# Kernel optimization log

Hardware: AMD Instinct MI355X
Metric: run time of the kernel (lower is better)

Reference implementation:

```python
import jax, jax.numpy as jnp
import numpy as np

N_NODES = 20000
N_EDGES = 80000
D = 128       # in_dim_node == in_dim_edge == hidden dims
ITERS = 15    # mp_iterations
EPS = 1e-5    # torch LayerNorm default eps


def _mlp(h, W0, b0, W1, b1, W2, b2, gamma, beta):
    """Linear-ReLU-Linear-ReLU-Linear-LayerNorm (hidden_layers=2)."""
    h = jax.nn.relu(h @ W0 + b0)
    h = jax.nn.relu(h @ W1 + b1)
    h = h @ W2 + b2
    mu = jnp.mean(h, axis=-1, keepdims=True)
    var = jnp.var(h, axis=-1, keepdims=True)
    return gamma * (h - mu) * jax.lax.rsqrt(var + EPS) + beta


def setup_inputs() -> dict:
    key = jax.random.key(0)
    ks = iter(jax.random.split(key, 32))

    def lin(fi, fo):
        bnd = 1.0 / np.sqrt(fi)
        W = jax.random.uniform(next(ks), (ITERS, fi, fo), minval=-bnd, maxval=bnd, dtype=jnp.float32)
        b = jax.random.uniform(next(ks), (ITERS, fo), minval=-bnd, maxval=bnd, dtype=jnp.float32)
        return W, b

    x = jax.random.normal(next(ks), (N_NODES, D), dtype=jnp.float32)
    edge_attr = jax.random.normal(next(ks), (N_EDGES, D), dtype=jnp.float32)
    edge_index = jax.random.randint(next(ks), (2, N_EDGES), 0, N_NODES)

    eW0, eB0 = lin(3 * D, D)   # edge MLP input = cat(src, dest, edge) = 384
    eW1, eB1 = lin(D, D)
    eW2, eB2 = lin(D, D)
    nW0, nB0 = lin(2 * D, D)   # node MLP input = cat(x, agg) = 256
    nW1, nB1 = lin(D, D)
    nW2, nB2 = lin(D, D)
    ones = jnp.ones((ITERS, D), jnp.float32)
    zeros = jnp.zeros((ITERS, D), jnp.float32)

    return dict(x=x, edge_attr=edge_attr,
                eW0=eW0, eB0=eB0, eW1=eW1, eB1=eB1, eW2=eW2, eB2=eB2, eG=ones, eBeta=zeros,
                nW0=nW0, nB0=nB0, nW1=nW1, nB1=nB1, nW2=nW2, nB2=nB2, nG=ones, nBeta=zeros,
                edge_index=edge_index)


def reference(x, edge_attr, eW0, eB0, eW1, eB1, eW2, eB2, eG, eBeta,
              nW0, nB0, nW1, nB1, nW2, nB2, nG, nBeta, edge_index):
    row, col = edge_index[0], edge_index[1]
    n = x.shape[0]
    params = (eW0, eB0, eW1, eB1, eW2, eB2, eG, eBeta,
              nW0, nB0, nW1, nB1, nW2, nB2, nG, nBeta)

    def step(carry, p):
        xc, ec = carry
        (ew0, eb0, ew1, eb1, ew2, eb2, eg, ebt,
         nw0, nb0, nw1, nb1, nw2, nb2, ng, nbt) = p
        # EdgeProcessor: gather + MLP, then FullResidualConnection (add previous)
        e_in = jnp.concatenate([xc[row], xc[col], ec], axis=-1)        # [E, 3D]
        ec = _mlp(e_in, ew0, eb0, ew1, eb1, ew2, eb2, eg, ebt) + ec
        # NodeProcessor: scatter_sum over destination nodes + MLP + residual
        agg = jax.ops.segment_sum(ec, col, num_segments=n)             # [N, D]
        n_in = jnp.concatenate([xc, agg], axis=-1)                     # [N, 2D]
        xc = _mlp(n_in, nw0, nb0, nw1, nb1, nw2, nb2, ng, nbt) + xc
        return (xc, ec), None

    (x, edge_attr), _ = jax.lax.scan(step, (x, edge_attr), params)
    return x, edge_attr
```

## Files before the change

### kernel.cpp

```cpp
#include <hip/hip_runtime.h>
#include <hip/hip_bf16.h>

typedef __hip_bfloat16 bf16;
typedef __attribute__((ext_vector_type(8))) short short8;
typedef __attribute__((ext_vector_type(4))) float f32x4;

#define NN 20000
#define NE 80000
#define DD 128
#define NITER 15
#define HSTRIDE 136

__device__ inline void gload16(const void* g, void* l) {
  __builtin_amdgcn_global_load_lds(
      (const __attribute__((address_space(1))) void*)g,
      (__attribute__((address_space(3))) void*)l, 16, 0, 0);
}

__device__ inline float bfbits2f(unsigned int hi16) {
  union { unsigned int u; float f; } c; c.u = hi16; return c.f;
}

__global__ void detect_kernel(const unsigned short* __restrict__ p, int nhalf,
                              int* __restrict__ flag) {
  __shared__ int cs[256], ct[256];
  const int t = threadIdx.x;
  int sane = 0, tot = 0;
  for (int i = 2 * t; i < nhalf; i += 512) {
    unsigned short v = p[i];
    int e = (v >> 7) & 0xFF;
    tot++;
    if (v == 0 || (e >= 80 && e <= 170)) sane++;
  }
  cs[t] = sane; ct[t] = tot;
  __syncthreads();
  for (int o = 128; o > 0; o >>= 1) {
    if (t < o) { cs[t] += cs[t + o]; ct[t] += ct[t + o]; }
    __syncthreads();
  }
  if (t == 0) *flag = (cs[0] * 10 > ct[0] * 7) ? 1 : 0;
}

__global__ void in2fb_kernel(const void* __restrict__ src, float* __restrict__ dstf,
                             bf16* __restrict__ dstb, int n, const int* __restrict__ flag) {
  int i = blockIdx.x * 256 + threadIdx.x;
  if (i < n) {
    float v = (*flag) ? (float)((const bf16*)src)[i] : ((const float*)src)[i];
    dstf[i] = v;
    dstb[i] = (bf16)v;
  }
}

__global__ void in2f_kernel(const void* __restrict__ src, float* __restrict__ dst,
                            int n, const int* __restrict__ flag) {
  int i = blockIdx.x * 256 + threadIdx.x;
  if (i < n) {
    dst[i] = (*flag) ? (float)((const bf16*)src)[i] : ((const float*)src)[i];
  }
}

__global__ void w2t_kernel(const void* __restrict__ W, bf16* __restrict__ Wt,
                           int K, const int* __restrict__ flag) {
  int i = blockIdx.x * 256 + threadIdx.x;
  int total = NITER * K * DD;
  if (i < total) {
    float v = (*flag) ? (float)((const bf16*)W)[i] : ((const float*)W)[i];
    int t = i / (K * DD);
    int rem = i - t * K * DD;
    int k = rem >> 7;
    int n = rem & 127;
    Wt[(size_t)t * K * DD + (size_t)n * K + k] = (bf16)v;
  }
}

__global__ void outw_kernel(const float* __restrict__ xf, const float* __restrict__ ef,
                            void* __restrict__ out, const int* __restrict__ flag) {
  int i = blockIdx.x * 256 + threadIdx.x;
  const int nx = NN * DD, total = (NN + NE) * DD;
  if (i < total) {
    float v = (i < nx) ? xf[i] : ef[i - nx];
    if (*flag) ((bf16*)out)[i] = (bf16)v;
    else       ((float*)out)[i] = v;
  }
}

template<int K0, int AMODE>
__global__ __launch_bounds__(256, 3) void fused_mlp(
    const bf16*  __restrict__ S0b,
    const bf16*  __restrict__ S1b,
    const int*   __restrict__ eidx,
    const bf16*  __restrict__ W0t,
    const bf16*  __restrict__ W1t,
    const bf16*  __restrict__ W2t,
    const float* __restrict__ b0,
    const float* __restrict__ b1,
    const float* __restrict__ b2,
    const float* __restrict__ gamma,
    const float* __restrict__ beta,
    float*       __restrict__ stf,
    bf16*        __restrict__ stb,
    int M)
{
  __shared__ __align__(16) bf16 Bls[2][128 * 32];
  __shared__ __align__(16) bf16 Hls[128 * HSTRIDE];

  const int tid  = threadIdx.x;
  const int lane = tid & 63;
  const int wv   = tid >> 6;
  const int l15  = lane & 15, quad = lane >> 4;
  const int m0   = blockIdx.x * 128;

  const int scol = tid >> 2;
  const int sk8  = (tid & 3) * 8;

  int rowm[2], ir[2], ic[2];
#pragma unroll
  for (int mi = 0; mi < 2; mi++) {
    rowm[mi] = min(m0 + wv * 32 + mi * 16 + l15, M - 1);
    if (AMODE == 1) { ir[mi] = eidx[rowm[mi]]; ic[mi] = eidx[NE + rowm[mi]]; }
  }

  auto dmaW = [&](const bf16* W, int K, int kk, int buf) {
    gload16(W + (size_t)scol * K + kk + sk8,        &Bls[buf][scol * 32 + sk8]);
    gload16(W + (size_t)(scol + 64) * K + kk + sk8, &Bls[buf][(scol + 64) * 32 + sk8]);
  };
  auto gatherA = [&](int kk, short8 a[2]) {
    const int ks = (kk & 127) + quad * 8;
#pragma unroll
    for (int mi = 0; mi < 2; mi++) {
      const bf16* base;
      if (AMODE == 1) {
        const int seg = kk >> 7;
        base = (seg == 0) ? S0b + (size_t)ir[mi] * DD
             : (seg == 1) ? S0b + (size_t)ic[mi] * DD
                          : S1b + (size_t)rowm[mi] * DD;
      } else {
        base = (kk >> 7) ? S1b + (size_t)rowm[mi] * DD
                         : S0b + (size_t)rowm[mi] * DD;
      }
      a[mi] = *(const short8*)(base + ks);
    }
  };

  f32x4 acc[2][8];
  auto zacc = [&]() {
#pragma unroll
    for (int i = 0; i < 2; i++)
#pragma unroll
      for (int j = 0; j < 8; j++) acc[i][j] = (f32x4){0.f, 0.f, 0.f, 0.f};
  };
  auto slabMfmaA = [&](const short8 a[2], int buf) {
    short8 bfr[8];
#pragma unroll
    for (int ni = 0; ni < 8; ni++)
      bfr[ni] = *(const short8*)&Bls[buf][(ni * 16 + l15) * 32 + quad * 8];
#pragma unroll
    for (int mi = 0; mi < 2; mi++)
#pragma unroll
      for (int ni = 0; ni < 8; ni++)
        acc[mi][ni] = __builtin_amdgcn_mfma_f32_16x16x32_bf16(a[mi], bfr[ni], acc[mi][ni], 0, 0, 0);
  };
  auto slabMfmaH = [&](int kk, int buf) {
    short8 a[2], bfr[8];
#pragma unroll
    for (int mi = 0; mi < 2; mi++)
      a[mi] = *(const short8*)&Hls[(wv * 32 + mi * 16 + l15) * HSTRIDE + kk + quad * 8];
#pragma unroll
    for (int ni = 0; ni < 8; ni++)
      bfr[ni] = *(const short8*)&Bls[buf][(ni * 16 + l15) * 32 + quad * 8];
#pragma unroll
    for (int mi = 0; mi < 2; mi++)
#pragma unroll
      for (int ni = 0; ni < 8; ni++)
        acc[mi][ni] = __builtin_amdgcn_mfma_f32_16x16x32_bf16(a[mi], bfr[ni], acc[mi][ni], 0, 0, 0);
  };
  auto writeH = [&](const float* bias) {
    float bv[8];
#pragma unroll
    for (int ni = 0; ni < 8; ni++) bv[ni] = bias[ni * 16 + l15];
#pragma unroll
    for (int mi = 0; mi < 2; mi++)
#pragma unroll
      for (int r = 0; r < 4; r++) {
        const int row = wv * 32 + mi * 16 + quad * 4 + r;
#pragma unroll
        for (int ni = 0; ni < 8; ni++)
          Hls[row * HSTRIDE + ni * 16 + l15] = (bf16)fmaxf(acc[mi][ni][r] + bv[ni], 0.f);
      }
  };

  constexpr int NS1 = K0 / 32;

  zacc();
  short8 aCur[2], aNxt[2];
  dmaW(W0t, K0, 0, 0);
  gatherA(0, aCur);
  __syncthreads();
#pragma unroll
  for (int s = 0; s < NS1; s++) {
    if (s + 1 < NS1) {
      dmaW(W0t, K0, (s + 1) * 32, (s + 1) & 1);
      gatherA((s + 1) * 32, aNxt);
    } else {
      dmaW(W1t, 128, 0, NS1 & 1);
    }
    slabMfmaA(aCur, s & 1);
    __syncthreads();
    aCur[0] = aNxt[0]; aCur[1] = aNxt[1];
  }
  writeH(b0);
  __syncthreads();

  zacc();
#pragma unroll
  for (int s = 0; s < 4; s++) {
    if (s < 3) dmaW(W1t, 128, (s + 1) * 32, (NS1 + s + 1) & 1);
    else       dmaW(W2t, 128, 0,            (NS1 + 4) & 1);
    slabMfmaH(s * 32, (NS1 + s) & 1);
    __syncthreads();
  }
  writeH(b1);
  __syncthreads();

  zacc();
#pragma unroll
  for (int s = 0; s < 4; s++) {
    if (s < 3) dmaW(W2t, 128, (s + 1) * 32, (NS1 + 4 + s + 1) & 1);
    slabMfmaH(s * 32, (NS1 + 4 + s) & 1);
    if (s < 3) __syncthreads();
  }

  float bv[8], gv[8], btv[8];
#pragma unroll
  for (int ni = 0; ni < 8; ni++) {
    const int col = ni * 16 + l15;
    bv[ni] = b2[col]; gv[ni] = gamma[col]; btv[ni] = beta[col];
  }
#pragma unroll
  for (int mi = 0; mi < 2; mi++)
#pragma unroll
    for (int r = 0; r < 4; r++) {
      float a = 0.f, bq = 0.f;
#pragma unroll
      for (int ni = 0; ni < 8; ni++) {
        const float v = acc[mi][ni][r] + bv[ni];
        a += v; bq += v * v;
      }
#pragma unroll
      for (int off = 1; off < 16; off <<= 1) {
        a  += __shfl_xor(a, off);
        bq += __shfl_xor(bq, off);
      }
      const float mu = a * (1.0f / 128.0f);
      const float var = fmaxf(bq * (1.0f / 128.0f) - mu * mu, 0.0f);
      const float rs = rsqrtf(var + 1e-5f);
      const int m = m0 + wv * 32 + mi * 16 + quad * 4 + r;
      if (m < M) {
#pragma unroll
        for (int ni = 0; ni < 8; ni++) {
          const int col = ni * 16 + l15;
          const float v = acc[mi][ni][r] + bv[ni];
          const float lnv = (v - mu) * rs * gv[ni] + btv[ni];
          const size_t idx = (size_t)m * DD + col;
          const float nv = lnv + stf[idx];
          stf[idx] = nv;
          stb[idx] = (bf16)nv;
        }
      }
    }
}

__global__ void zero_kernel(int* __restrict__ p, int n) {
  int i = blockIdx.x * 256 + threadIdx.x;
  if (i < n) p[i] = 0;
}

__global__ void hist_kernel(const int* __restrict__ eidx, int* __restrict__ counts) {
  int e = blockIdx.x * 256 + threadIdx.x;
  if (e < NE) atomicAdd(&counts[eidx[NE + e]], 1);
}

__global__ void scan_kernel(const int* __restrict__ counts, int* __restrict__ offs,
                            int* __restrict__ cursor) {
  __shared__ int sums[1024];
  const int t = threadIdx.x;
  const int base = t * 20;
  int local[20];
  int s = 0;
  for (int i = 0; i < 20; i++) {
    int idx = base + i;
    int c = (idx < NN) ? counts[idx] : 0;
    local[i] = s; s += c;
  }
  sums[t] = s;
  __syncthreads();
  for (int off = 1; off < 1024; off <<= 1) {
    int v = 0;
    if (t >= off) v = sums[t - off];
    __syncthreads();
    if (t >= off) sums[t] += v;
    __syncthreads();
  }
  int excl = (t == 0) ? 0 : sums[t - 1];
  for (int i = 0; i < 20; i++) {
    int idx = base + i;
    if (idx < NN) { offs[idx] = excl + local[i]; cursor[idx] = 0; }
  }
  if (t == 1023) offs[NN] = sums[1023];
}

__global__ void fill_kernel(const int* __restrict__ eidx, const int* __restrict__ offs,
                            int* __restrict__ cursor, int* __restrict__ sorted) {
  int e = blockIdx.x * 256 + threadIdx.x;
  if (e < NE) {
    int n = eidx[NE + e];
    int p = atomicAdd(&cursor[n], 1);
    sorted[offs[n] + p] = e;
  }
}

__global__ void aggregate_kernel(const bf16* __restrict__ eb, const int* __restrict__ offs,
                                 const int* __restrict__ sorted, bf16* __restrict__ aggb) {
  const int node = blockIdx.x * 4 + (threadIdx.x >> 6);
  const int lane = threadIdx.x & 63;
  if (node >= NN) return;
  const int s = offs[node], t = offs[node + 1];
  float a0 = 0.f, a1 = 0.f;
  for (int i = s; i < t; i++) {
    const int e = sorted[i];
    unsigned int v = *(const unsigned int*)(eb + (size_t)e * DD + 2 * lane);
    a0 += bfbits2f(v << 16);
    a1 += bfbits2f(v & 0xFFFF0000u);
  }
  bf16 o0 = (bf16)a0, o1 = (bf16)a1;
  unsigned int pack = (unsigned int)(*(unsigned short*)&o0)
                    | ((unsigned int)(*(unsigned short*)&o1) << 16);
  *(unsigned int*)(aggb + (size_t)node * DD + 2 * lane) = pack;
}

extern "C" void kernel_launch(void* const* d_in, const int* in_sizes, int n_in,
                              void* d_out, int out_size, void* d_ws, size_t ws_size,
                              hipStream_t stream) {
  const void* x_in = d_in[0];
  const void* e_in = d_in[1];
  const void* eW0 = d_in[2];
  const void* eB0 = d_in[3];
  const void* eW1 = d_in[4];
  const void* eB1 = d_in[5];
  const void* eW2 = d_in[6];
  const void* eB2 = d_in[7];
  const void* eG  = d_in[8];
  const void* eBt = d_in[9];
  const void* nW0 = d_in[10];
  const void* nB0 = d_in[11];
  const void* nW1 = d_in[12];
  const void* nB1 = d_in[13];
  const void* nW2 = d_in[14];
  const void* nB2 = d_in[15];
  const void* nG  = d_in[16];
  const void* nBt = d_in[17];
  const int*  eidx = (const int*)d_in[18];

  char* ws = (char*)d_ws;
  size_t off = 0;
  auto alloc = [&](size_t bytes) -> char* {
    char* p = ws + off;
    off = (off + bytes + 255) & ~(size_t)255;
    return p;
  };

  float* xf   = (float*)alloc((size_t)NN * DD * 4);
  float* ef   = (float*)alloc((size_t)NE * DD * 4);
  bf16*  xb   = (bf16*)alloc((size_t)NN * DD * 2);
  bf16*  eb   = (bf16*)alloc((size_t)NE * DD * 2);
  bf16*  aggb = (bf16*)alloc((size_t)NN * DD * 2);
  bf16*  eW0t = (bf16*)alloc((size_t)NITER * 384 * DD * 2);
  bf16*  eW1t = (bf16*)alloc((size_t)NITER * 128 * DD * 2);
  bf16*  eW2t = (bf16*)alloc((size_t)NITER * 128 * DD * 2);
  bf16*  nW0t = (bf16*)alloc((size_t)NITER * 256 * DD * 2);
  bf16*  nW1t = (bf16*)alloc((size_t)NITER * 128 * DD * 2);
  bf16*  nW2t = (bf16*)alloc((size_t)NITER * 128 * DD * 2);
  const int NB = NITER * DD;
  float* eB0f = (float*)alloc(NB * 4);
  float* eB1f = (float*)alloc(NB * 4);
  float* eB2f = (float*)alloc(NB * 4);
  float* eGf  = (float*)alloc(NB * 4);
  float* eBtf = (float*)alloc(NB * 4);
  float* nB0f = (float*)alloc(NB * 4);
  float* nB1f = (float*)alloc(NB * 4);
  float* nB2f = (float*)alloc(NB * 4);
  float* nGf  = (float*)alloc(NB * 4);
  float* nBtf = (float*)alloc(NB * 4);
  int* counts = (int*)alloc((size_t)NN * 4);
  int* cursor = (int*)alloc((size_t)NN * 4);
  int* offs   = (int*)alloc((size_t)(NN + 1) * 4);
  int* sorted = (int*)alloc((size_t)NE * 4);
  int* flag   = (int*)alloc(4);

  detect_kernel<<<1, 256, 0, stream>>>((const unsigned short*)x_in, 16384, flag);

  in2fb_kernel<<<(NN * DD + 255) / 256, 256, 0, stream>>>(x_in, xf, xb, NN * DD, flag);
  in2fb_kernel<<<(NE * DD + 255) / 256, 256, 0, stream>>>(e_in, ef, eb, NE * DD, flag);
  w2t_kernel<<<(NITER * 384 * DD + 255) / 256, 256, 0, stream>>>(eW0, eW0t, 384, flag);
  w2t_kernel<<<(NITER * 128 * DD + 255) / 256, 256, 0, stream>>>(eW1, eW1t, 128, flag);
  w2t_kernel<<<(NITER * 128 * DD + 255) / 256, 256, 0, stream>>>(eW2, eW2t, 128, flag);
  w2t_kernel<<<(NITER * 256 * DD + 255) / 256, 256, 0, stream>>>(nW0, nW0t, 256, flag);
  w2t_kernel<<<(NITER * 128 * DD + 255) / 256, 256, 0, stream>>>(nW1, nW1t, 128, flag);
  w2t_kernel<<<(NITER * 128 * DD + 255) / 256, 256, 0, stream>>>(nW2, nW2t, 128, flag);
  in2f_kernel<<<(NB + 255) / 256, 256, 0, stream>>>(eB0, eB0f, NB, flag);
  in2f_kernel<<<(NB + 255) / 256, 256, 0, stream>>>(eB1, eB1f, NB, flag);
  in2f_kernel<<<(NB + 255) / 256, 256, 0, stream>>>(eB2, eB2f, NB, flag);
  in2f_kernel<<<(NB + 255) / 256, 256, 0, stream>>>(eG,  eGf,  NB, flag);
  in2f_kernel<<<(NB + 255) / 256, 256, 0, stream>>>(eBt, eBtf, NB, flag);
  in2f_kernel<<<(NB + 255) / 256, 256, 0, stream>>>(nB0, nB0f, NB, flag);
  in2f_kernel<<<(NB + 255) / 256, 256, 0, stream>>>(nB1, nB1f, NB, flag);
  in2f_kernel<<<(NB + 255) / 256, 256, 0, stream>>>(nB2, nB2f, NB, flag);
  in2f_kernel<<<(NB + 255) / 256, 256, 0, stream>>>(nG,  nGf,  NB, flag);
  in2f_kernel<<<(NB + 255) / 256, 256, 0, stream>>>(nBt, nBtf, NB, flag);

  zero_kernel<<<(NN + 255) / 256, 256, 0, stream>>>(counts, NN);
  hist_kernel<<<(NE + 255) / 256, 256, 0, stream>>>(eidx, counts);
  scan_kernel<<<1, 1024, 0, stream>>>(counts, offs, cursor);
  fill_kernel<<<(NE + 255) / 256, 256, 0, stream>>>(eidx, offs, cursor, sorted);

  const int egrid = NE / 128;
  const int ngrid = (NN + 127) / 128;

  for (int t = 0; t < NITER; t++) {
    fused_mlp<384, 1><<<egrid, 256, 0, stream>>>(
        xb, eb, eidx,
        eW0t + (size_t)t * 384 * DD, eW1t + (size_t)t * 128 * DD, eW2t + (size_t)t * 128 * DD,
        eB0f + t * DD, eB1f + t * DD, eB2f + t * DD,
        eGf + t * DD, eBtf + t * DD, ef, eb, NE);
    aggregate_kernel<<<(NN + 3) / 4, 256, 0, stream>>>(eb, offs, sorted, aggb);
    fused_mlp<256, 2><<<ngrid, 256, 0, stream>>>(
        xb, aggb, nullptr,
        nW0t + (size_t)t * 256 * DD, nW1t + (size_t)t * 128 * DD, nW2t + (size_t)t * 128 * DD,
        nB0f + t * DD, nB1f + t * DD, nB2f + t * DD,
        nGf + t * DD, nBtf + t * DD, xf, xb, NN);
  }

  outw_kernel<<<((NN + NE) * DD + 255) / 256, 256, 0, stream>>>(xf, ef, d_out, flag);
}
```

Baseline: 1.295 ms.

## Fuse aggregation into node MLP, drop fp32 residual state, merge preprocessing kernels

```diff
diff --git a/kernel.cpp b/kernel.cpp
--- a/kernel.cpp
+++ b/kernel.cpp
@@ -21,13 +21,22 @@
   union { unsigned int u; float f; } c; c.u = hi16; return c.f;
 }
 
-__global__ void detect_kernel(const unsigned short* __restrict__ p, int nhalf,
-                              int* __restrict__ flag) {
+__device__ inline float readin(const void* p, int i, int fl) {
+  return fl ? (float)((const bf16*)p)[i] : ((const float*)p)[i];
+}
+
+__global__ void detzero_kernel(const unsigned short* __restrict__ x,
+                               int* __restrict__ counts, int* __restrict__ flag) {
+  const int bid = blockIdx.x, t = threadIdx.x;
+  if (bid < 79) {
+    int i = bid * 256 + t;
+    if (i < NN) counts[i] = 0;
+    return;
+  }
   __shared__ int cs[256], ct[256];
-  const int t = threadIdx.x;
   int sane = 0, tot = 0;
-  for (int i = 2 * t; i < nhalf; i += 512) {
-    unsigned short v = p[i];
+  for (int i = 2 * t; i < 16384; i += 512) {
+    unsigned short v = x[i];
     int e = (v >> 7) & 0xFF;
     tot++;
     if (v == 0 || (e >= 80 && e <= 170)) sane++;
@@ -41,66 +50,69 @@
   if (t == 0) *flag = (cs[0] * 10 > ct[0] * 7) ? 1 : 0;
 }
 
-__global__ void in2fb_kernel(const void* __restrict__ src, float* __restrict__ dstf,
-                             bf16* __restrict__ dstb, int n, const int* __restrict__ flag) {
-  int i = blockIdx.x * 256 + threadIdx.x;
-  if (i < n) {
-    float v = (*flag) ? (float)((const bf16*)src)[i] : ((const float*)src)[i];
-    dstf[i] = v;
-    dstb[i] = (bf16)v;
-  }
-}
-
-__global__ void in2f_kernel(const void* __restrict__ src, float* __restrict__ dst,
-                            int n, const int* __restrict__ flag) {
-  int i = blockIdx.x * 256 + threadIdx.x;
-  if (i < n) {
-    dst[i] = (*flag) ? (float)((const bf16*)src)[i] : ((const float*)src)[i];
-  }
-}
-
-__global__ void w2t_kernel(const void* __restrict__ W, bf16* __restrict__ Wt,
-                           int K, const int* __restrict__ flag) {
-  int i = blockIdx.x * 256 + threadIdx.x;
-  int total = NITER * K * DD;
-  if (i < total) {
-    float v = (*flag) ? (float)((const bf16*)W)[i] : ((const float*)W)[i];
-    int t = i / (K * DD);
-    int rem = i - t * K * DD;
-    int k = rem >> 7;
-    int n = rem & 127;
-    Wt[(size_t)t * K * DD + (size_t)n * K + k] = (bf16)v;
-  }
-}
-
-__global__ void outw_kernel(const float* __restrict__ xf, const float* __restrict__ ef,
-                            void* __restrict__ out, const int* __restrict__ flag) {
-  int i = blockIdx.x * 256 + threadIdx.x;
-  const int nx = NN * DD, total = (NN + NE) * DD;
-  if (i < total) {
-    float v = (i < nx) ? xf[i] : ef[i - nx];
-    if (*flag) ((bf16*)out)[i] = (bf16)v;
-    else       ((float*)out)[i] = v;
-  }
-}
-
-template<int K0, int AMODE>
-__global__ __launch_bounds__(256, 3) void fused_mlp(
-    const bf16*  __restrict__ S0b,
-    const bf16*  __restrict__ S1b,
-    const int*   __restrict__ eidx,
-    const bf16*  __restrict__ W0t,
-    const bf16*  __restrict__ W1t,
-    const bf16*  __restrict__ W2t,
-    const float* __restrict__ b0,
-    const float* __restrict__ b1,
+#define CX  (NN * DD)
+#define CE  (NE * DD)
+#define CW0 (NITER * 384 * DD)
+#define CW1 (NITER * 128 * DD)
+#define CNW0 (NITER * 256 * DD)
+#define CB  (NITER * DD)
+#define BX0 CX
+#define BX1 (BX0 + CE)
+#define BX7 (BX1 + CW0 + CW1 + CW1 + CNW0 + CW1 + CW1)
+#define BX8 (BX7 + 10 * CB)
+
+struct CvtP {
+  const void *x, *e;
+  const void* w[6];
+  bf16 *xb, *eb;
+  bf16* wt[6];
+  const void* bs[10];
+  float* bd[10];
+  const int* flag;
+};
+
+__global__ void convert_all(CvtP P) {
+  const int fl = *P.flag;
+  const int gstride = gridDim.x * 256;
+  for (int i = blockIdx.x * 256 + threadIdx.x; i < BX8; i += gstride) {
+    if (i < BX0) {
+      P.xb[i] = (bf16)readin(P.x, i, fl);
+    } else if (i < BX1) {
+      P.eb[i - BX0] = (bf16)readin(P.e, i - BX0, fl);
+    } else if (i < BX7) {
+      int j = i - BX1, w;
+      if (j < CW0) { w = 0; }
+      else if ((j -= CW0) < CW1) { w = 1; }
+      else if ((j -= CW1) < CW1) { w = 2; }
+      else if ((j -= CW1) < CNW0) { w = 3; }
+      else if ((j -= CNW0) < CW1) { w = 4; }
+      else { j -= CW1; w = 5; }
+      const int K = (w == 0) ? 384 : (w == 3) ? 256 : 128;
+      float v = readin(P.w[w], j, fl);
+      int it = j / (K * DD);
+      int rem = j - it * K * DD;
+      int k = rem >> 7, n = rem & 127;
+      P.wt[w][(size_t)it * K * DD + (size_t)n * K + k] = (bf16)v;
+    } else {
+      int j = i - BX7;
+      int b = j / CB, r = j - b * CB;
+      P.bd[b][r] = readin(P.bs[b], r, fl);
+    }
+  }
+}
+
+__global__ __launch_bounds__(256, 3) void edge_mlp(
+    const bf16* __restrict__ xb,
+    const bf16* eb,
+    const int*  __restrict__ eidx,
+    const bf16* __restrict__ W0t, const bf16* __restrict__ W1t,
+    const bf16* __restrict__ W2t,
+    const float* __restrict__ b0, const float* __restrict__ b1,
     const float* __restrict__ b2,
-    const float* __restrict__ gamma,
-    const float* __restrict__ beta,
-    float*       __restrict__ stf,
-    bf16*        __restrict__ stb,
-    int M)
+    const float* __restrict__ gamma, const float* __restrict__ beta,
+    bf16* st, int M)
 {
+  constexpr int K0 = 384, NS1 = 12;
   __shared__ __align__(16) bf16 Bls[2][128 * 32];
   __shared__ __align__(16) bf16 Hls[128 * HSTRIDE];
 
@@ -109,7 +121,6 @@
   const int wv   = tid >> 6;
   const int l15  = lane & 15, quad = lane >> 4;
   const int m0   = blockIdx.x * 128;
-
   const int scol = tid >> 2;
   const int sk8  = (tid & 3) * 8;
 
@@ -117,7 +128,7 @@
 #pragma unroll
   for (int mi = 0; mi < 2; mi++) {
     rowm[mi] = min(m0 + wv * 32 + mi * 16 + l15, M - 1);
-    if (AMODE == 1) { ir[mi] = eidx[rowm[mi]]; ic[mi] = eidx[NE + rowm[mi]]; }
+    ir[mi] = eidx[rowm[mi]]; ic[mi] = eidx[NE + rowm[mi]];
   }
 
   auto dmaW = [&](const bf16* W, int K, int kk, int buf) {
@@ -128,16 +139,10 @@
     const int ks = (kk & 127) + quad * 8;
 #pragma unroll
     for (int mi = 0; mi < 2; mi++) {
-      const bf16* base;
-      if (AMODE == 1) {
-        const int seg = kk >> 7;
-        base = (seg == 0) ? S0b + (size_t)ir[mi] * DD
-             : (seg == 1) ? S0b + (size_t)ic[mi] * DD
-                          : S1b + (size_t)rowm[mi] * DD;
-      } else {
-        base = (kk >> 7) ? S1b + (size_t)rowm[mi] * DD
-                         : S0b + (size_t)rowm[mi] * DD;
-      }
+      const int seg = kk >> 7;
+      const bf16* base = (seg == 0) ? xb + (size_t)ir[mi] * DD
+                       : (seg == 1) ? xb + (size_t)ic[mi] * DD
+                                    : eb + (size_t)rowm[mi] * DD;
       a[mi] = *(const short8*)(base + ks);
     }
   };
@@ -188,8 +193,6 @@
           Hls[row * HSTRIDE + ni * 16 + l15] = (bf16)fmaxf(acc[mi][ni][r] + bv[ni], 0.f);
       }
   };
-
-  constexpr int NS1 = K0 / 32;
 
   zacc();
   short8 aCur[2], aNxt[2];
@@ -262,17 +265,176 @@
           const float v = acc[mi][ni][r] + bv[ni];
           const float lnv = (v - mu) * rs * gv[ni] + btv[ni];
           const size_t idx = (size_t)m * DD + col;
-          const float nv = lnv + stf[idx];
-          stf[idx] = nv;
-          stb[idx] = (bf16)nv;
+          st[idx] = (bf16)(lnv + (float)st[idx]);
         }
       }
     }
 }
 
-__global__ void zero_kernel(int* __restrict__ p, int n) {
-  int i = blockIdx.x * 256 + threadIdx.x;
-  if (i < n) p[i] = 0;
+__global__ __launch_bounds__(256, 4) void node_mlp(
+    const bf16* xb,
+    const bf16* __restrict__ eb,
+    const int*  __restrict__ offs,
+    const int*  __restrict__ sorted,
+    const bf16* __restrict__ W0t, const bf16* __restrict__ W1t,
+    const bf16* __restrict__ W2t,
+    const float* __restrict__ b0, const float* __restrict__ b1,
+    const float* __restrict__ b2,
+    const float* __restrict__ gamma, const float* __restrict__ beta,
+    bf16* st, int M)
+{
+  constexpr int K0 = 256, NS1 = 8;
+  __shared__ __align__(16) bf16 Bls[2][128 * 32];
+  __shared__ __align__(16) bf16 Hls[64 * HSTRIDE];
+
+  const int tid  = threadIdx.x;
+  const int lane = tid & 63;
+  const int wv   = tid >> 6;
+  const int l15  = lane & 15, quad = lane >> 4;
+  const int m0   = blockIdx.x * 64;
+  const int scol = tid >> 2;
+  const int sk8  = (tid & 3) * 8;
+
+  for (int j = 0; j < 16; j++) {
+    const int n = m0 + wv * 16 + j;
+    if (n < M) {
+      const int s = offs[n], e2 = offs[n + 1];
+      float a0 = 0.f, a1 = 0.f;
+      for (int i = s; i < e2; i++) {
+        const int e = sorted[i];
+        unsigned int v = *(const unsigned int*)(eb + (size_t)e * DD + 2 * lane);
+        a0 += bfbits2f(v << 16);
+        a1 += bfbits2f(v & 0xFFFF0000u);
+      }
+      bf16 o0 = (bf16)a0, o1 = (bf16)a1;
+      unsigned int pack = (unsigned int)(*(unsigned short*)&o0)
+                        | ((unsigned int)(*(unsigned short*)&o1) << 16);
+      *(unsigned int*)&Hls[(wv * 16 + j) * HSTRIDE + 2 * lane] = pack;
+    }
+  }
+
+  const int rowm = min(m0 + wv * 16 + l15, M - 1);
+
+  auto dmaW = [&](const bf16* W, int K, int kk, int buf) {
+    gload16(W + (size_t)scol * K + kk + sk8,        &Bls[buf][scol * 32 + sk8]);
+    gload16(W + (size_t)(scol + 64) * K + kk + sk8, &Bls[buf][(scol + 64) * 32 + sk8]);
+  };
+  auto gatherA = [&](int kk, short8* a) {
+    const int ks = (kk & 127) + quad * 8;
+    if (kk < 128) *a = *(const short8*)(xb + (size_t)rowm * DD + ks);
+    else          *a = *(const short8*)&Hls[(rowm - m0) * HSTRIDE + ks];
+  };
+
+  f32x4 acc[8];
+  auto zacc = [&]() {
+#pragma unroll
+    for (int j = 0; j < 8; j++) acc[j] = (f32x4){0.f, 0.f, 0.f, 0.f};
+  };
+  auto slabMfmaA = [&](short8 a, int buf) {
+    short8 bfr[8];
+#pragma unroll
+    for (int ni = 0; ni < 8; ni++)
+      bfr[ni] = *(const short8*)&Bls[buf][(ni * 16 + l15) * 32 + quad * 8];
+#pragma unroll
+    for (int ni = 0; ni < 8; ni++)
+      acc[ni] = __builtin_amdgcn_mfma_f32_16x16x32_bf16(a, bfr[ni], acc[ni], 0, 0, 0);
+  };
+  auto slabMfmaH = [&](int kk, int buf) {
+    short8 a = *(const short8*)&Hls[(wv * 16 + l15) * HSTRIDE + kk + quad * 8];
+    short8 bfr[8];
+#pragma unroll
+    for (int ni = 0; ni < 8; ni++)
+      bfr[ni] = *(const short8*)&Bls[buf][(ni * 16 + l15) * 32 + quad * 8];
+#pragma unroll
+    for (int ni = 0; ni < 8; ni++)
+      acc[ni] = __builtin_amdgcn_mfma_f32_16x16x32_bf16(a, bfr[ni], acc[ni], 0, 0, 0);
+  };
+  auto writeH = [&](const float* bias) {
+    float bv[8];
+#pragma unroll
+    for (int ni = 0; ni < 8; ni++) bv[ni] = bias[ni * 16 + l15];
+#pragma unroll
+    for (int r = 0; r < 4; r++) {
+      const int row = wv * 16 + quad * 4 + r;
+#pragma unroll
+      for (int ni = 0; ni < 8; ni++)
+        Hls[row * HSTRIDE + ni * 16 + l15] = (bf16)fmaxf(acc[ni][r] + bv[ni], 0.f);
+    }
+  };
+
+  zacc();
+  short8 aCur, aNxt;
+  dmaW(W0t, K0, 0, 0);
+  gatherA(0, &aCur);
+  __syncthreads();
+#pragma unroll
+  for (int s = 0; s < NS1; s++) {
+    if (s + 1 < NS1) {
+      dmaW(W0t, K0, (s + 1) * 32, (s + 1) & 1);
+      gatherA((s + 1) * 32, &aNxt);
+    } else {
+      dmaW(W1t, 128, 0, NS1 & 1);
+    }
+    slabMfmaA(aCur, s & 1);
+    __syncthreads();
+    aCur = aNxt;
+  }
+  writeH(b0);
+  __syncthreads();
+
+  zacc();
+#pragma unroll
+  for (int s = 0; s < 4; s++) {
+    if (s < 3) dmaW(W1t, 128, (s + 1) * 32, (NS1 + s + 1) & 1);
+    else       dmaW(W2t, 128, 0,            (NS1 + 4) & 1);
+    slabMfmaH(s * 32, (NS1 + s) & 1);
+    __syncthreads();
+  }
+  writeH(b1);
+  __syncthreads();
+
+  zacc();
+#pragma unroll
+  for (int s = 0; s < 4; s++) {
+    if (s < 3) dmaW(W2t, 128, (s + 1) * 32, (NS1 + 4 + s + 1) & 1);
+    slabMfmaH(s * 32, (NS1 + 4 + s) & 1);
+    if (s < 3) __syncthreads();
+  }
+
+  float bv[8], gv[8], btv[8];
+#pragma unroll
+  for (int ni = 0; ni < 8; ni++) {
+    const int col = ni * 16 + l15;
+    bv[ni] = b2[col]; gv[ni] = gamma[col]; btv[ni] = beta[col];
+  }
+#pragma unroll
+  for (int r = 0; r < 4; r++) {
+    float a = 0.f, bq = 0.f;
+#pragma unroll
+    for (int ni = 0; ni < 8; ni++) {
+      const float v = acc[ni][r] + bv[ni];
+      a += v; bq += v * v;
+    }
+#pragma unroll
+    for (int off = 1; off < 16; off <<= 1) {
+      a  += __shfl_xor(a, off);
+      bq += __shfl_xor(bq, off);
+    }
+    const float mu = a * (1.0f / 128.0f);
+    const float var = fmaxf(bq * (1.0f / 128.0f) - mu * mu, 0.0f);
+    const float rs = rsqrtf(var + 1e-5f);
+    const int m = m0 + wv * 16 + quad * 4 + r;
+    if (m < M) {
+#pragma unroll
+      for (int ni = 0; ni < 8; ni++) {
+        const int col = ni * 16 + l15;
+        const float v = acc[ni][r] + bv[ni];
+        const float lnv = (v - mu) * rs * gv[ni] + btv[ni];
+        const size_t idx = (size_t)m * DD + col;
+        st[idx] = (bf16)(lnv + (float)st[idx]);
+      }
+    }
+  }
 }
 
 __global__ void hist_kernel(const int* __restrict__ eidx, int* __restrict__ counts) {
@@ -319,47 +481,21 @@
   }
 }
 
-__global__ void aggregate_kernel(const bf16* __restrict__ eb, const int* __restrict__ offs,
-                                 const int* __restrict__ sorted, bf16* __restrict__ aggb) {
-  const int node = blockIdx.x * 4 + (threadIdx.x >> 6);
-  const int lane = threadIdx.x & 63;
-  if (node >= NN) return;
-  const int s = offs[node], t = offs[node + 1];
-  float a0 = 0.f, a1 = 0.f;
-  for (int i = s; i < t; i++) {
-    const int e = sorted[i];
-    unsigned int v = *(const unsigned int*)(eb + (size_t)e * DD + 2 * lane);
-    a0 += bfbits2f(v << 16);
-    a1 += bfbits2f(v & 0xFFFF0000u);
-  }
-  bf16 o0 = (bf16)a0, o1 = (bf16)a1;
-  unsigned int pack = (unsigned int)(*(unsigned short*)&o0)
-                    | ((unsigned int)(*(unsigned short*)&o1) << 16);
-  *(unsigned int*)(aggb + (size_t)node * DD + 2 * lane) = pack;
+__global__ void outwb_kernel(const bf16* __restrict__ xb, const bf16* __restrict__ eb,
+                             void* __restrict__ out, const int* __restrict__ flag) {
+  int i = blockIdx.x * 256 + threadIdx.x;
+  const int nx = NN * DD, total = (NN + NE) * DD;
+  if (i < total) {
+    bf16 v = (i < nx) ? xb[i] : eb[i - nx];
+    if (*flag) ((bf16*)out)[i] = v;
+    else       ((float*)out)[i] = (float)v;
+  }
 }
 
 extern "C" void kernel_launch(void* const* d_in, const int* in_sizes, int n_in,
                               void* d_out, int out_size, void* d_ws, size_t ws_size,
                               hipStream_t stream) {
-  const void* x_in = d_in[0];
-  const void* e_in = d_in[1];
-  const void* eW0 = d_in[2];
-  const void* eB0 = d_in[3];
-  const void* eW1 = d_in[4];
-  const void* eB1 = d_in[5];
-  const void* eW2 = d_in[6];
-  const void* eB2 = d_in[7];
-  const void* eG  = d_in[8];
-  const void* eBt = d_in[9];
-  const void* nW0 = d_in[10];
-  const void* nB0 = d_in[11];
-  const void* nW1 = d_in[12];
-  const void* nB1 = d_in[13];
-  const void* nW2 = d_in[14];
-  const void* nB2 = d_in[15];
-  const void* nG  = d_in[16];
-  const void* nBt = d_in[17];
-  const int*  eidx = (const int*)d_in[18];
+  const int* eidx = (const int*)d_in[18];
 
   char* ws = (char*)d_ws;
   size_t off = 0;
@@ -369,76 +505,57 @@
     return p;
   };
 
-  float* xf   = (float*)alloc((size_t)NN * DD * 4);
-  float* ef   = (float*)alloc((size_t)NE * DD * 4);
-  bf16*  xb   = (bf16*)alloc((size_t)NN * DD * 2);
-  bf16*  eb   = (bf16*)alloc((size_t)NE * DD * 2);
-  bf16*  aggb = (bf16*)alloc((size_t)NN * DD * 2);
-  bf16*  eW0t = (bf16*)alloc((size_t)NITER * 384 * DD * 2);
-  bf16*  eW1t = (bf16*)alloc((size_t)NITER * 128 * DD * 2);
-  bf16*  eW2t = (bf16*)alloc((size_t)NITER * 128 * DD * 2);
-  bf16*  nW0t = (bf16*)alloc((size_t)NITER * 256 * DD * 2);
-  bf16*  nW1t = (bf16*)alloc((size_t)NITER * 128 * DD * 2);
-  bf16*  nW2t = (bf16*)alloc((size_t)NITER * 128 * DD * 2);
-  const int NB = NITER * DD;
-  float* eB0f = (float*)alloc(NB * 4);
-  float* eB1f = (float*)alloc(NB * 4);
-  float* eB2f = (float*)alloc(NB * 4);
-  float* eGf  = (float*)alloc(NB * 4);
-  float* eBtf = (float*)alloc(NB * 4);
-  float* nB0f = (float*)alloc(NB * 4);
-  float* nB1f = (float*)alloc(NB * 4);
-  float* nB2f = (float*)alloc(NB * 4);
-  float* nGf  = (float*)alloc(NB * 4);
-  float* nBtf = (float*)alloc(NB * 4);
+  bf16* xb   = (bf16*)alloc((size_t)NN * DD * 2);
+  bf16* eb   = (bf16*)alloc((size_t)NE * DD * 2);
+  bf16* eW0t = (bf16*)alloc((size_t)CW0 * 2);
+  bf16* eW1t = (bf16*)alloc((size_t)CW1 * 2);
+  bf16* eW2t = (bf16*)alloc((size_t)CW1 * 2);
+  bf16* nW0t = (bf16*)alloc((size_t)CNW0 * 2);
+  bf16* nW1t = (bf16*)alloc((size_t)CW1 * 2);
+  bf16* nW2t = (bf16*)alloc((size_t)CW1 * 2);
+  float* bf_[10];
+  for (int i = 0; i < 10; i++) bf_[i] = (float*)alloc(CB * 4);
   int* counts = (int*)alloc((size_t)NN * 4);
   int* cursor = (int*)alloc((size_t)NN * 4);
   int* offs   = (int*)alloc((size_t)(NN + 1) * 4);
   int* sorted = (int*)alloc((size_t)NE * 4);
   int* flag   = (int*)alloc(4);
 
-  detect_kernel<<<1, 256, 0, stream>>>((const unsigned short*)x_in, 16384, flag);
-
-  in2fb_kernel<<<(NN * DD + 255) / 256, 256, 0, stream>>>(x_in, xf, xb, NN * DD, flag);
-  in2fb_kernel<<<(NE * DD + 255) / 256, 256, 0, stream>>>(e_in, ef, eb, NE * DD, flag);
-  w2t_kernel<<<(NITER * 384 * DD + 255) / 256, 256, 0, stream>>>(eW0, eW0t, 384, flag);
-  w2t_kernel<<<(NITER * 128 * DD + 255) / 256, 256, 0, stream>>>(eW1, eW1t, 128, flag);
-  w2t_kernel<<<(NITER * 128 * DD + 255) / 256, 256, 0, stream>>>(eW2, eW2t, 128, flag);
-  w2t_kernel<<<(NITER * 256 * DD + 255) / 256, 256, 0, stream>>>(nW0, nW0t, 256, flag);
-  w2t_kernel<<<(NITER * 128 * DD + 255) / 256, 256, 0, stream>>>(nW1, nW1t, 128, flag);
-  w2t_kernel<<<(NITER * 128 * DD + 255) / 256, 256, 0, stream>>>(nW2, nW2t, 128, flag);
-  in2f_kernel<<<(NB + 255) / 256, 256, 0, stream>>>(eB0, eB0f, NB, flag);
-  in2f_kernel<<<(NB + 255) / 256, 256, 0, stream>>>(eB1, eB1f, NB, flag);
-  in2f_kernel<<<(NB + 255) / 256, 256, 0, stream>>>(eB2, eB2f, NB, flag);
-  in2f_kernel<<<(NB + 255) / 256, 256, 0, stream>>>(eG,  eGf,  NB, flag);
-  in2f_kernel<<<(NB + 255) / 256, 256, 0, stream>>>(eBt, eBtf, NB, flag);
-  in2f_kernel<<<(NB + 255) / 256, 256, 0, stream>>>(nB0, nB0f, NB, flag);
-  in2f_kernel<<<(NB + 255) / 256, 256, 0, stream>>>(nB1, nB1f, NB, flag);
-  in2f_kernel<<<(NB + 255) / 256, 256, 0, stream>>>(nB2, nB2f, NB, flag);
-  in2f_kernel<<<(NB + 255) / 256, 256, 0, stream>>>(nG,  nGf,  NB, flag);
-  in2f_kernel<<<(NB + 255) / 256, 256, 0, stream>>>(nBt, nBtf, NB, flag);
-
-  zero_kernel<<<(NN + 255) / 256, 256, 0, stream>>>(counts, NN);
+  detzero_kernel<<<80, 256, 0, stream>>>((const unsigned short*)d_in[0], counts, flag);
+
+  CvtP C;
+  C.x = d_in[0]; C.e = d_in[1];
+  C.w[0] = d_in[2];  C.w[1] = d_in[4];  C.w[2] = d_in[6];
+  C.w[3] = d_in[10]; C.w[4] = d_in[12]; C.w[5] = d_in[14];
+  C.xb = xb; C.eb = eb;
+  C.wt[0] = eW0t; C.wt[1] = eW1t; C.wt[2] = eW2t;
+  C.wt[3] = nW0t; C.wt[4] = nW1t; C.wt[5] = nW2t;
+  const int bsrc_idx[10] = {3, 5, 7, 8, 9, 11, 13, 15, 16, 17};
+  for (int i = 0; i < 10; i++) { C.bs[i] = d_in[bsrc_idx[i]]; C.bd[i] = bf_[i]; }
+  C.flag = flag;
+  convert_all<<<2048, 256, 0, stream>>>(C);
+
   hist_kernel<<<(NE + 255) / 256, 256, 0, stream>>>(eidx, counts);
   scan_kernel<<<1, 1024, 0, stream>>>(counts, offs, cursor);
   fill_kernel<<<(NE + 255) / 256, 256, 0, stream>>>(eidx, offs, cursor, sorted);
 
   const int egrid = NE / 128;
-  const int ngrid = (NN + 127) / 128;
+  const int ngrid = (NN + 63) / 64;
 
   for (int t = 0; t < NITER; t++) {
-    fused_mlp<384, 1><<<egrid, 256, 0, stream>>>(
+    edge_mlp<<<egrid, 256, 0, stream>>>(
         xb, eb, eidx,
-        eW0t + (size_t)t * 384 * DD, eW1t + (size_t)t * 128 * DD, eW2t + (size_t)t * 128 * DD,
-        eB0f + t * DD, eB1f + t * DD, eB2f + t * DD,
-        eGf + t * DD, eBtf + t * DD, ef, eb, NE);
-    aggregate_kernel<<<(NN + 3) / 4, 256, 0, stream>>>(eb, offs, sorted, aggb);
-    fused_mlp<256, 2><<<ngrid, 256, 0, stream>>>(
-        xb, aggb, nullptr,
-        nW0t + (size_t)t * 256 * DD, nW1t + (size_t)t * 128 * DD, nW2t + (size_t)t * 128 * DD,
-        nB0f + t * DD, nB1f + t * DD, nB2f + t * DD,
-        nGf + t * DD, nBtf + t * DD, xf, xb, NN);
-  }
-
-  outw_kernel<<<((NN + NE) * DD + 255) / 256, 256, 0, stream>>>(xf, ef, d_out, flag);
-}
+        eW0t + (size_t)t * 384 * DD, eW1t + (size_t)t * 128 * DD,
+        eW2t + (size_t)t * 128 * DD,
+        bf_[0] + t * DD, bf_[1] + t * DD, bf_[2] + t * DD,
+        bf_[3] + t * DD, bf_[4] + t * DD, eb, NE);
+    node_mlp<<<ngrid, 256, 0, stream>>>(
+        xb, eb, offs, sorted,
+        nW0t + (size_t)t * 256 * DD, nW1t + (size_t)t * 128 * DD,
+        nW2t + (size_t)t * 128 * DD,
+        bf_[5] + t * DD, bf_[6] + t * DD, bf_[7] + t * DD,
+        bf_[8] + t * DD, bf_[9] + t * DD, xb, NN);
+  }
+
+  outwb_kernel<<<((NN + NE) * DD + 255) / 256, 256, 0, stream>>>(xb, eb, d_out, flag);
+}
```

New measurement: 1.509 ms. 16.5% more time.
